# Kernel tuning notes

Hardware: AMD Instinct MI355X
Metric: run time of the kernel (lower is better)

Reference implementation:

```python
import jax, jax.numpy as jnp
import numpy as np
import math

B, N = 1, 768
CS, CZ, CH, H, PQ, PV, E3 = 384, 128, 16, 12, 4, 8, 4
INF, EPS = 1e5, 1e-8


def _quat_to_rot(q):
    # q: [..., 4] unnormalized quaternion -> [..., 3, 3] rotation matrix
    q = q / jnp.linalg.norm(q, axis=-1, keepdims=True)
    w, x, y, z = q[..., 0], q[..., 1], q[..., 2], q[..., 3]
    R = jnp.stack([
        1 - 2 * (y * y + z * z), 2 * (x * y - w * z), 2 * (x * z + w * y),
        2 * (x * y + w * z), 1 - 2 * (x * x + z * z), 2 * (y * z - w * x),
        2 * (x * z - w * y), 2 * (y * z + w * x), 1 - 2 * (x * x + y * y),
    ], axis=-1)
    return R.reshape(q.shape[:-1] + (3, 3))


def setup_inputs() -> dict:
    key = jax.random.key(0)
    ks = jax.random.split(key, 24)
    hc = H * CH
    hpq = H * PQ * 3
    hpkv = H * (PQ + PV) * 3
    cod = CZ // 4 + CH + PV * 4  # 80
    def w(k, shape, fan_in):
        return jax.random.normal(k, shape, jnp.float32) / math.sqrt(fan_in)
    inp = {
        "s": jax.random.normal(ks[0], (B, N, CS), jnp.float32),
        "z": jax.random.normal(ks[1], (B, N, N, CZ), jnp.float32),
        "l1_feats": jax.random.normal(ks[2], (B, N, E3 * 3), jnp.float32),
        "rot": _quat_to_rot(jax.random.normal(ks[3], (B, N, 4), jnp.float32)),
        "trans": jax.random.normal(ks[4], (B, N, 3), jnp.float32),
        "mask": jnp.ones((B, N), jnp.float32),
        "Wq": w(ks[5], (hc, CS), CS), "bq": jnp.zeros((hc,), jnp.float32),
        "Wkv": w(ks[6], (2 * hc, CS), CS), "bkv": jnp.zeros((2 * hc,), jnp.float32),
        "Wqp": w(ks[7], (hpq, CS), CS), "bqp": jnp.zeros((hpq,), jnp.float32),
        "Wkvp": w(ks[8], (hpkv, CS), CS), "bkvp": jnp.zeros((hpkv,), jnp.float32),
        "Wb": w(ks[9], (H, CZ), CZ), "bb": jnp.zeros((H,), jnp.float32),
        "Wdz": w(ks[10], (CZ // 4, CZ), CZ), "bdz": jnp.zeros((CZ // 4,), jnp.float32),
        "Wout": w(ks[11], (CS, H * cod), H * cod), "bout": jnp.zeros((CS,), jnp.float32),
        "Wl1": jax.random.normal(ks[12], (H * PV, E3), jnp.float32),
    }
    return inp


def _split3(x):
    # torch.split(x, d//3, -1) then stack(dim=-1): [..., 3*P] -> [..., P, 3]
    return jnp.swapaxes(x.reshape(x.shape[:-1] + (3, -1)), -1, -2)


def reference(s, z, l1_feats, rot, trans, mask,
              Wq, bq, Wkv, bkv, Wqp, bqp, Wkvp, bkvp,
              Wb, bb, Wdz, bdz, Wout, bout, Wl1):
    s_org = s
    q = (s @ Wq.T + bq).reshape(B, N, H, CH)
    kv = (s @ Wkv.T + bkv).reshape(B, N, H, 2 * CH)
    k, v = kv[..., :CH], kv[..., CH:]

    # points in global frame: R p + t
    q_pts = _split3(s @ Wqp.T + bqp)                      # [B,N,H*PQ,3]
    q_pts = jnp.einsum("bnij,bnpj->bnpi", rot, q_pts) + trans[:, :, None, :]
    q_pts = q_pts.reshape(B, N, H, PQ, 3)
    kv_pts = _split3(s @ Wkvp.T + bkvp)                   # [B,N,H*(PQ+PV),3]
    kv_pts = jnp.einsum("bnij,bnpj->bnpi", rot, kv_pts) + trans[:, :, None, :]
    kv_pts = kv_pts.reshape(B, N, H, PQ + PV, 3)
    k_pts, v_pts = kv_pts[..., :PQ, :], kv_pts[..., PQ:, :]

    b = z @ Wb.T + bb                                     # [B,N,N,H]
    a = math.sqrt(1.0 / (3 * CH)) * jnp.einsum("bihc,bjhc->bhij", q, k)
    a = a + math.sqrt(1.0 / 3) * jnp.transpose(b, (0, 3, 1, 2))

    diff = q_pts[:, :, None] - k_pts[:, None]             # [B,N,N,H,PQ,3]
    pt_att = -0.5 * jnp.sum(diff * diff, axis=(-1, -2))   # [B,N,N,H]
    a = a + jnp.transpose(pt_att, (0, 3, 1, 2))

    sq_mask = INF * (mask[:, :, None] * mask[:, None, :] - 1.0)
    a = jax.nn.softmax(a + sq_mask[:, None], axis=-1)     # [B,H,N,N]

    o = jnp.einsum("bhij,bjhc->bihc", a, v).reshape(B, N, H * CH)
    o_pt = jnp.einsum("bhij,bjhpc->bihpc", a, v_pts)      # [B,N,H,PV,3] (global frame)

    # e3nn o3.Linear on (H*PV)x1o -> E3x1o: per-xyz channel mixing / sqrt(fan_in)
    o_pt_l1 = o_pt.reshape(B, N, H * PV, 3)
    l1_out = l1_feats + (jnp.einsum("bnic,io->bnoc", o_pt_l1, Wl1)
                         / math.sqrt(H * PV)).reshape(B, N, E3 * 3)

    # back to local frame: R^T (p - t)
    o_pt_loc = jnp.einsum("bnji,bnhpj->bnhpi", rot,
                          o_pt - trans[:, :, None, None, :])
    o_pt_dists = jnp.sqrt(jnp.sum(o_pt_loc ** 2, axis=-1) + EPS).reshape(B, N, H * PV)
    o_pt_flat = o_pt_loc.reshape(B, N, H * PV, 3)

    pair_z = z @ Wdz.T + bdz                              # [B,N,N,CZ//4]
    o_pair = jnp.einsum("bhij,bijd->bihd", a, pair_z).reshape(B, N, H * (CZ // 4))

    feats = jnp.concatenate([o, o_pt_flat[..., 0], o_pt_flat[..., 1],
                             o_pt_flat[..., 2], o_pt_dists, o_pair], axis=-1)
    s_out = feats @ Wout.T + bout + s_org
    return s_out, l1_out
```

## Files before the change

### kernel.cpp

```cpp
#include <hip/hip_runtime.h>

#define INFV 100000.0f
#define CQK 0.14433756729740643f
#define CB  0.5773502691896258f
#define INV_SQRT96 0.10206207261596577f

typedef short bf16x8 __attribute__((ext_vector_type(8)));
typedef float f32x4 __attribute__((ext_vector_type(4)));

#define OFF_WT    0
#define OFF_WOT   442368
#define OFF_BU    811008
#define OFF_Q     812160
#define OFF_KH    959616
#define OFF_KPH   1107072
#define OFF_QP    1217664
#define OFF_BM    1328256
#define OFF_A     4867200
#define OFF_VCT   8406144
#define OFF_PZ    8627328
#define OFF_O     18064512
#define OFF_OPT   18211968
#define OFF_OPAIR 18433152
#define OFF_ZB    18728064
#define OFF_WC    18728068
#define OFF_BC    18731140

static __device__ __forceinline__ unsigned short f2bf(float x) {
  unsigned int u = __float_as_uint(x);
  unsigned int r = (u + 0x7fffu + ((u >> 16) & 1u)) >> 16;
  return (unsigned short)r;
}
static __device__ __forceinline__ float bf2f(unsigned short b) {
  return __uint_as_float(((unsigned int)b) << 16);
}

__global__ __launch_bounds__(256) void kT(
    const float* __restrict__ Wq, const float* __restrict__ Wkv,
    const float* __restrict__ Wqp, const float* __restrict__ Wkvp,
    const float* __restrict__ Wout,
    const float* __restrict__ bq, const float* __restrict__ bkv,
    const float* __restrict__ bqp, const float* __restrict__ bkvp,
    const float* __restrict__ Wb, const float* __restrict__ bb,
    const float* __restrict__ Wdz, const float* __restrict__ bdz,
    float* __restrict__ WT, float* __restrict__ WoutT, float* __restrict__ bu,
    unsigned short* __restrict__ vcT, float* __restrict__ zb,
    unsigned short* __restrict__ Wc, float* __restrict__ biasc) {
  int tid = blockIdx.x * 256 + threadIdx.x;
  if (tid < 442368) {
    int f = tid / 1152, u = tid % 1152;
    float w;
    if (u < 192)      w = Wq[u * 384 + f];
    else if (u < 576) w = Wkv[(u - 192) * 384 + f];
    else if (u < 720) w = Wqp[(u - 576) * 384 + f];
    else              w = Wkvp[(u - 720) * 384 + f];
    WT[tid] = w;
  } else if (tid < 811008) {
    int r = tid - 442368;
    int f = r / 384, o = r % 384;
    WoutT[r] = Wout[o * 960 + f];
  } else if (tid < 812160) {
    int u = tid - 811008;
    float bv;
    if (u < 192)      bv = bq[u];
    else if (u < 576) bv = bkv[u - 192];
    else if (u < 720) bv = bqp[u - 576];
    else              bv = bkvp[u - 720];
    bu[u] = bv;
  } else if (tid < 849024) {
    int zid = tid - 812160;
    int h = zid / 3072, r = zid % 3072;
    ((unsigned int*)(vcT + h * 36864 + 40 * 768))[r] = 0u;
  } else if (tid < 849028) {
    ((unsigned int*)zb)[tid - 849024] = 0u;
  } else if (tid < 855172) {
    int wid = tid - 849028;
    int n = wid >> 7, k = wid & 127;
    float val = (n < 12) ? CB * Wb[n * 128 + k] : ((n < 44) ? Wdz[(n - 12) * 128 + k] : 0.f);
    Wc[wid] = f2bf(val);
  } else if (tid < 855220) {
    int n = tid - 855172;
    biasc[n] = (n < 12) ? CB * bb[n] : ((n < 44) ? bdz[n - 12] : 0.f);
  }
}

__global__ __launch_bounds__(384) void kA(
    const float* __restrict__ s, const float* __restrict__ rot, const float* __restrict__ trans,
    const float* __restrict__ WT, const float* __restrict__ bu,
    float* __restrict__ q, float* __restrict__ kh, float* __restrict__ kph,
    float* __restrict__ qp, unsigned short* __restrict__ vcT) {
  __shared__ float sA[4][384];
  __shared__ float praw[4][576];
  const int t = threadIdx.x;
  const int n0 = blockIdx.x * 4;
  for (int idx = t; idx < 4 * 384; idx += 384) sA[idx / 384][idx % 384] = s[n0 * 384 + idx];
  __syncthreads();

  float acc[3][4];
#pragma unroll
  for (int a = 0; a < 3; a++)
#pragma unroll
    for (int r = 0; r < 4; r++) acc[a][r] = 0.f;
  const int u0 = t, u1 = t + 384, u2 = t + 768;

  for (int f = 0; f < 384; f += 4) {
    float4 sr0 = *(const float4*)&sA[0][f];
    float4 sr1 = *(const float4*)&sA[1][f];
    float4 sr2 = *(const float4*)&sA[2][f];
    float4 sr3 = *(const float4*)&sA[3][f];
#pragma unroll
    for (int ff = 0; ff < 4; ff++) {
      const float* wrow = WT + (size_t)(f + ff) * 1152;
      float w0 = wrow[u0], w1 = wrow[u1], w2 = wrow[u2];
      float v0 = ((const float*)&sr0)[ff];
      float v1 = ((const float*)&sr1)[ff];
      float v2 = ((const float*)&sr2)[ff];
      float v3 = ((const float*)&sr3)[ff];
      acc[0][0] = fmaf(w0, v0, acc[0][0]); acc[0][1] = fmaf(w0, v1, acc[0][1]);
      acc[0][2] = fmaf(w0, v2, acc[0][2]); acc[0][3] = fmaf(w0, v3, acc[0][3]);
      acc[1][0] = fmaf(w1, v0, acc[1][0]); acc[1][1] = fmaf(w1, v1, acc[1][1]);
      acc[1][2] = fmaf(w1, v2, acc[1][2]); acc[1][3] = fmaf(w1, v3, acc[1][3]);
      acc[2][0] = fmaf(w2, v0, acc[2][0]); acc[2][1] = fmaf(w2, v1, acc[2][1]);
      acc[2][2] = fmaf(w2, v2, acc[2][2]); acc[2][3] = fmaf(w2, v3, acc[2][3]);
    }
  }

#pragma unroll
  for (int a = 0; a < 3; a++) {
    int u = t + a * 384;
    float bv = bu[u];
#pragma unroll
    for (int r = 0; r < 4; r++) {
      float val = acc[a][r] + bv;
      int n = n0 + r;
      if (u < 192) {
        q[n * 192 + u] = val;
      } else if (u < 576) {
        int l = u - 192, h = l >> 5, rem = l & 31;
        if (rem < 16) kh[h * 12288 + n * 16 + rem] = val;
        else          vcT[h * 36864 + (rem - 16) * 768 + n] = f2bf(val);
      } else {
        praw[r][u - 576] = val;
      }
    }
  }
  __syncthreads();

  for (int task = t; task < 4 * 192; task += 384) {
    int r = task / 192, p = task % 192;
    int n = n0 + r;
    const float* R = rot + n * 9;
    const float* tr = trans + n * 3;
    float x, y, z;
    if (p < 48) {
      x = praw[r][p]; y = praw[r][48 + p]; z = praw[r][96 + p];
      int h = p >> 2, pq = p & 3;
      float* outp = qp + n * 144 + h * 12 + pq * 3;
      outp[0] = R[0] * x + R[1] * y + R[2] * z + tr[0];
      outp[1] = R[3] * x + R[4] * y + R[5] * z + tr[1];
      outp[2] = R[6] * x + R[7] * y + R[8] * z + tr[2];
    } else {
      int pp = p - 48;
      x = praw[r][144 + pp]; y = praw[r][288 + pp]; z = praw[r][432 + pp];
      int h = pp / 12, idx = pp % 12;
      float gx = R[0] * x + R[1] * y + R[2] * z + tr[0];
      float gy = R[3] * x + R[4] * y + R[5] * z + tr[1];
      float gz = R[6] * x + R[7] * y + R[8] * z + tr[2];
      if (idx < 4) {
        float* outp = kph + h * 9216 + n * 12 + idx * 3;
        outp[0] = gx; outp[1] = gy; outp[2] = gz;
      } else {
        int pv = idx - 4;
        unsigned short* vb = vcT + h * 36864 + (16 + pv * 3) * 768 + n;
        vb[0] = f2bf(gx); vb[768] = f2bf(gy); vb[1536] = f2bf(gz);
      }
    }
  }
}

__global__ __launch_bounds__(256) void kB2(
    const float* __restrict__ z, const unsigned short* __restrict__ Wc,
    const float* __restrict__ biasc,
    unsigned short* __restrict__ bm16, unsigned short* __restrict__ pz) {
  __shared__ unsigned short zL[64][136];
  __shared__ unsigned short wL[48][136];
  __shared__ unsigned short oD[64][48];
  __shared__ float biasL[48];
  const int t = threadIdx.x;
  const size_t pid0 = (size_t)blockIdx.x * 64;

  {
    const unsigned int* wsrc = (const unsigned int*)Wc;
#pragma unroll
    for (int it = 0; it < 12; it++) {
      int idx = it * 256 + t;
      int n = idx >> 6, col = (idx & 63) * 2;
      *(unsigned int*)&wL[n][col] = wsrc[idx];
    }
    if (t < 48) biasL[t] = biasc[t];
  }
  const float4* zsrc = (const float4*)(z + pid0 * 128);
#pragma unroll
  for (int it = 0; it < 8; it++) {
    int f4 = it * 256 + t;
    float4 v = zsrc[f4];
    int row = f4 >> 5, col = (f4 & 31) * 4;
    unsigned int p0 = (unsigned int)f2bf(v.x) | ((unsigned int)f2bf(v.y) << 16);
    unsigned int p1 = (unsigned int)f2bf(v.z) | ((unsigned int)f2bf(v.w) << 16);
    uint2 pk = make_uint2(p0, p1);
    *(uint2*)&zL[row][col] = pk;
  }
  __syncthreads();

  const int w = t >> 6, l = t & 63;
  const int lr = l & 15, hk = l >> 4;
  f32x4 acc0 = {0.f, 0.f, 0.f, 0.f}, acc1 = acc0, acc2 = acc0;
  const int arow = w * 16 + lr;
#pragma unroll
  for (int kc = 0; kc < 4; kc++) {
    int col = kc * 32 + hk * 8;
    bf16x8 af = *(const bf16x8*)&zL[arow][col];
    bf16x8 b0 = *(const bf16x8*)&wL[lr][col];
    bf16x8 b1 = *(const bf16x8*)&wL[16 + lr][col];
    bf16x8 b2 = *(const bf16x8*)&wL[32 + lr][col];
    acc0 = __builtin_amdgcn_mfma_f32_16x16x32_bf16(af, b0, acc0, 0, 0, 0);
    acc1 = __builtin_amdgcn_mfma_f32_16x16x32_bf16(af, b1, acc1, 0, 0, 0);
    acc2 = __builtin_amdgcn_mfma_f32_16x16x32_bf16(af, b2, acc2, 0, 0, 0);
  }
  {
    int rb = w * 16 + hk * 4;
#pragma unroll
    for (int r = 0; r < 4; r++) {
      oD[rb + r][lr]      = f2bf(acc0[r] + biasL[lr]);
      oD[rb + r][16 + lr] = f2bf(acc1[r] + biasL[16 + lr]);
      oD[rb + r][32 + lr] = f2bf(acc2[r] + biasL[32 + lr]);
    }
  }
  __syncthreads();

  {
    int row = t >> 2, qd = t & 3;
    uint2 lo = *(const uint2*)&oD[row][12 + qd * 8];
    uint2 hi = *(const uint2*)&oD[row][12 + qd * 8 + 4];
    uint4 val = make_uint4(lo.x, lo.y, hi.x, hi.y);
    *(uint4*)(pz + (pid0 + row) * 32 + qd * 8) = val;
  }
  for (int idx = t; idx < 384; idx += 256) {
    int h = idx / 32, pr = idx % 32;
    unsigned int u = (unsigned int)oD[2 * pr][h] | ((unsigned int)oD[2 * pr + 1][h] << 16);
    ((unsigned int*)(bm16 + (size_t)h * 589824 + pid0))[pr] = u;
  }
}

__global__ __launch_bounds__(256) void kC1(
    const float* __restrict__ q, const float* __restrict__ qp,
    const float* __restrict__ kh, const float* __restrict__ kph,
    const unsigned short* __restrict__ bm16, const float* __restrict__ mask,
    unsigned short* __restrict__ A) {
  __shared__ float lg[12 * 776];
  __shared__ float qL[192], qpL[144], maskL[768];
  __shared__ float mxL[12], ivL[12];
  const int t = threadIdx.x;
  const int i = blockIdx.x;
  for (int idx = t; idx < 192; idx += 256) qL[idx] = q[i * 192 + idx];
  for (int idx = t; idx < 144; idx += 256) qpL[idx] = qp[i * 144 + idx];
  for (int j = t; j < 768; j += 256) maskL[j] = mask[j];
  __syncthreads();
  const float mi = maskL[i];

  for (int h = 0; h < 12; h++) {
    const float4* qv = (const float4*)&qL[h * 16];
    float4 q0 = qv[0], q1 = qv[1], q2 = qv[2], q3 = qv[3];
    const float4* av = (const float4*)&qpL[h * 12];
    float4 a0 = av[0], a1 = av[1], a2 = av[2];
    for (int j = t; j < 768; j += 256) {
      const float4* kr = (const float4*)(kh + h * 12288 + j * 16);
      float4 k0 = kr[0], k1 = kr[1], k2 = kr[2], k3 = kr[3];
      const float4* pr = (const float4*)(kph + h * 9216 + j * 12);
      float4 p0 = pr[0], p1 = pr[1], p2 = pr[2];
      float bsc = bf2f(bm16[(size_t)h * 589824 + i * 768 + j]);
      float qk =
          q0.x * k0.x + q0.y * k0.y + q0.z * k0.z + q0.w * k0.w +
          q1.x * k1.x + q1.y * k1.y + q1.z * k1.z + q1.w * k1.w +
          q2.x * k2.x + q2.y * k2.y + q2.z * k2.z + q2.w * k2.w +
          q3.x * k3.x + q3.y * k3.y + q3.z * k3.z + q3.w * k3.w;
      float d, pt = 0.f;
      d = a0.x - p0.x; pt = fmaf(d, d, pt);
      d = a0.y - p0.y; pt = fmaf(d, d, pt);
      d = a0.z - p0.z; pt = fmaf(d, d, pt);
      d = a0.w - p0.w; pt = fmaf(d, d, pt);
      d = a1.x - p1.x; pt = fmaf(d, d, pt);
      d = a1.y - p1.y; pt = fmaf(d, d, pt);
      d = a1.z - p1.z; pt = fmaf(d, d, pt);
      d = a1.w - p1.w; pt = fmaf(d, d, pt);
      d = a2.x - p2.x; pt = fmaf(d, d, pt);
      d = a2.y - p2.y; pt = fmaf(d, d, pt);
      d = a2.z - p2.z; pt = fmaf(d, d, pt);
      d = a2.w - p2.w; pt = fmaf(d, d, pt);
      lg[h * 776 + j] = fmaf(CQK, qk, bsc) - 0.5f * pt + INFV * (mi * maskL[j] - 1.0f);
    }
  }
  __syncthreads();

  const int w = t >> 6, ln = t & 63;
  for (int h = w; h < 12; h += 4) {
    const float* row = lg + h * 776;
    float m = -3.0e38f;
#pragma unroll
    for (int kq = 0; kq < 12; kq++) m = fmaxf(m, row[ln + kq * 64]);
#pragma unroll
    for (int sh = 1; sh < 64; sh <<= 1) m = fmaxf(m, __shfl_xor(m, sh));
    float ssum = 0.f;
#pragma unroll
    for (int kq = 0; kq < 12; kq++) ssum += __expf(row[ln + kq * 64] - m);
#pragma unroll
    for (int sh = 1; sh < 64; sh <<= 1) ssum += __shfl_xor(ssum, sh);
    if (ln == 0) { mxL[h] = m; ivL[h] = 1.0f / ssum; }
  }
  __syncthreads();

  for (int idx = t; idx < 4608; idx += 256) {
    int h = idx / 384, jp = idx % 384;
    float m = mxL[h], iv = ivL[h];
    int j0 = jp * 2;
    float e0 = __expf(lg[h * 776 + j0] - m) * iv;
    float e1 = __expf(lg[h * 776 + j0 + 1] - m) * iv;
    unsigned int pk = (unsigned int)f2bf(e0) | ((unsigned int)f2bf(e1) << 16);
    ((unsigned int*)(A + (size_t)h * 589824 + i * 768))[jp] = pk;
  }
}

__global__ __launch_bounds__(128) void kC2(
    const unsigned short* __restrict__ A, const unsigned short* __restrict__ vcT,
    float* __restrict__ o_out, float* __restrict__ opt_out) {
  const int t = threadIdx.x;
  const int h = blockIdx.x % 12, it = blockIdx.x / 12;
  const int i0 = it * 32;
  const int w = t >> 6, l = t & 63;
  const int lr = l & 15, lk = (l >> 4) * 8;
  f32x4 acc0 = {0.f, 0.f, 0.f, 0.f}, acc1 = acc0, acc2 = acc0;
  const unsigned short* ab = A + (size_t)h * 589824 + (i0 + w * 16 + lr) * 768 + lk;
  const unsigned short* bb = vcT + h * 36864 + lr * 768 + lk;
#pragma unroll 4
  for (int kc = 0; kc < 24; kc++) {
    int k0 = kc * 32;
    bf16x8 avf = *(const bf16x8*)(ab + k0);
    bf16x8 b0 = *(const bf16x8*)(bb + k0);
    bf16x8 b1 = *(const bf16x8*)(bb + 16 * 768 + k0);
    bf16x8 b2 = *(const bf16x8*)(bb + 32 * 768 + k0);
    acc0 = __builtin_amdgcn_mfma_f32_16x16x32_bf16(avf, b0, acc0, 0, 0, 0);
    acc1 = __builtin_amdgcn_mfma_f32_16x16x32_bf16(avf, b1, acc1, 0, 0, 0);
    acc2 = __builtin_amdgcn_mfma_f32_16x16x32_bf16(avf, b2, acc2, 0, 0, 0);
  }
  const int rowb = i0 + w * 16 + (l >> 4) * 4;
#pragma unroll
  for (int r = 0; r < 4; r++) {
    int row = rowb + r;
    o_out[row * 192 + h * 16 + lr] = acc0[r];
    opt_out[row * 288 + h * 24 + lr] = acc1[r];
    if (lr < 8) opt_out[row * 288 + h * 24 + 16 + lr] = acc2[r];
  }
}

__global__ __launch_bounds__(256) void kC3(
    const unsigned short* __restrict__ A, const unsigned short* __restrict__ pz,
    const unsigned short* __restrict__ zb, float* __restrict__ opair_out) {
  __shared__ unsigned short pzT[32 * 776];
  __shared__ float red[4][16][33];
  const int t = threadIdx.x, i = blockIdx.x;

  unsigned int* pzU = (unsigned int*)pzT;
  for (int p = t; p < 384; p += 256) {
    const uint4* r0 = (const uint4*)(pz + (size_t)(i * 768 + 2 * p) * 32);
    union { uint4 v[8]; unsigned short u[64]; } rw;
#pragma unroll
    for (int c = 0; c < 8; c++) rw.v[c] = r0[c];
#pragma unroll
    for (int d = 0; d < 32; d++)
      pzU[d * 388 + p] = (unsigned int)rw.u[d] | ((unsigned int)rw.u[32 + d] << 16);
  }
  __syncthreads();

  const int w = t >> 6, l = t & 63;
  const int lr = l & 15, lk = (l >> 4) * 8;
  f32x4 acc0 = {0.f, 0.f, 0.f, 0.f}, acc1 = acc0;
  const unsigned short* abase = (lr < 12) ? (A + (size_t)lr * 589824 + i * 768 + lk) : zb;
  const int astep = (lr < 12) ? 1 : 0;
#pragma unroll
  for (int kc = 0; kc < 6; kc++) {
    int k0 = w * 192 + kc * 32;
    bf16x8 avf = *(const bf16x8*)(abase + astep * k0);
    bf16x8 b0 = *(const bf16x8*)(pzT + lr * 776 + k0 + lk);
    bf16x8 b1 = *(const bf16x8*)(pzT + (16 + lr) * 776 + k0 + lk);
    acc0 = __builtin_amdgcn_mfma_f32_16x16x32_bf16(avf, b0, acc0, 0, 0, 0);
    acc1 = __builtin_amdgcn_mfma_f32_16x16x32_bf16(avf, b1, acc1, 0, 0, 0);
  }
#pragma unroll
  for (int r = 0; r < 4; r++) {
    red[w][(l >> 4) * 4 + r][lr] = acc0[r];
    red[w][(l >> 4) * 4 + r][16 + lr] = acc1[r];
  }
  __syncthreads();
  for (int idx = t; idx < 512; idx += 256) {
    int row = idx >> 5, col = idx & 31;
    if (row < 12) {
      float sv = red[0][row][col] + red[1][row][col] + red[2][row][col] + red[3][row][col];
      opair_out[i * 384 + row * 32 + col] = sv;
    }
  }
}

__global__ __launch_bounds__(512) void kD(
    const float* __restrict__ o_in, const float* __restrict__ opt_in, const float* __restrict__ opair_in,
    const float* __restrict__ rot, const float* __restrict__ trans,
    const float* __restrict__ l1f, const float* __restrict__ Wl1,
    const float* __restrict__ WoutT, const float* __restrict__ bout,
    const float* __restrict__ s_org, float* __restrict__ out) {
  __shared__ float feats[4][960];
  __shared__ float part[2][256][6];
  const int t = threadIdx.x;
  const int n0 = blockIdx.x * 4;

  for (int idx = t; idx < 768; idx += 512) feats[idx / 192][idx % 192] = o_in[n0 * 192 + idx];
  for (int idx = t; idx < 1536; idx += 512) feats[idx / 384][576 + idx % 384] = opair_in[n0 * 384 + idx];
  if (t < 384) {
    int r = t / 96, p = t % 96, n = n0 + r;
    float x = opt_in[n * 288 + p * 3 + 0];
    float y = opt_in[n * 288 + p * 3 + 1];
    float zc = opt_in[n * 288 + p * 3 + 2];
    const float* R = rot + n * 9;
    const float* tr = trans + n * 3;
    float dx = x - tr[0], dy = y - tr[1], dz = zc - tr[2];
    float l0 = R[0] * dx + R[3] * dy + R[6] * dz;
    float l1 = R[1] * dx + R[4] * dy + R[7] * dz;
    float l2 = R[2] * dx + R[5] * dy + R[8] * dz;
    feats[r][192 + p] = l0;
    feats[r][288 + p] = l1;
    feats[r][384 + p] = l2;
    feats[r][480 + p] = sqrtf(l0 * l0 + l1 * l1 + l2 * l2 + 1e-8f);
  } else if (t < 432) {
    int tt = t - 384, r = tt / 12, lq = tt % 12, n = n0 + r;
    int oo = lq / 3, cc = lq % 3;
    float acc = 0.f;
    for (int i = 0; i < 96; i++) acc = fmaf(opt_in[n * 288 + i * 3 + cc], Wl1[i * 4 + oo], acc);
    out[294912 + n * 12 + lq] = l1f[n * 12 + lq] + acc * INV_SQRT96;
  }
  __syncthreads();

  const int fh = t >> 8, tt = t & 255;
  const int o0 = tt & 127, rp = tt >> 7;
  float acc[3][2] = {{0.f, 0.f}, {0.f, 0.f}, {0.f, 0.f}};
  for (int f = fh * 480; f < fh * 480 + 480; f++) {
    float w0 = WoutT[f * 384 + o0];
    float w1 = WoutT[f * 384 + o0 + 128];
    float w2 = WoutT[f * 384 + o0 + 256];
    float s0 = feats[rp * 2][f], s1 = feats[rp * 2 + 1][f];
    acc[0][0] = fmaf(w0, s0, acc[0][0]); acc[0][1] = fmaf(w0, s1, acc[0][1]);
    acc[1][0] = fmaf(w1, s0, acc[1][0]); acc[1][1] = fmaf(w1, s1, acc[1][1]);
    acc[2][0] = fmaf(w2, s0, acc[2][0]); acc[2][1] = fmaf(w2, s1, acc[2][1]);
  }
#pragma unroll
  for (int kq = 0; kq < 3; kq++)
#pragma unroll
    for (int r = 0; r < 2; r++) part[fh][tt][kq * 2 + r] = acc[kq][r];
  __syncthreads();
  if (t < 256) {
    const int ob = t & 127, rb = t >> 7;
#pragma unroll
    for (int kq = 0; kq < 3; kq++) {
      int o = ob + kq * 128;
#pragma unroll
      for (int r = 0; r < 2; r++) {
        int n = n0 + rb * 2 + r;
        float v = part[0][t][kq * 2 + r] + part[1][t][kq * 2 + r] + bout[o] + s_org[n * 384 + o];
        out[n * 384 + o] = v;
      }
    }
  }
}

extern "C" void kernel_launch(void* const* d_in, const int* in_sizes, int n_in,
                              void* d_out, int out_size, void* d_ws, size_t ws_size,
                              hipStream_t stream) {
  (void)in_sizes; (void)n_in; (void)out_size; (void)ws_size;
  const float* s     = (const float*)d_in[0];
  const float* z     = (const float*)d_in[1];
  const float* l1f   = (const float*)d_in[2];
  const float* rot   = (const float*)d_in[3];
  const float* trans = (const float*)d_in[4];
  const float* mask  = (const float*)d_in[5];
  const float* Wq    = (const float*)d_in[6];
  const float* bq    = (const float*)d_in[7];
  const float* Wkv   = (const float*)d_in[8];
  const float* bkv   = (const float*)d_in[9];
  const float* Wqp   = (const float*)d_in[10];
  const float* bqp   = (const float*)d_in[11];
  const float* Wkvp  = (const float*)d_in[12];
  const float* bkvp  = (const float*)d_in[13];
  const float* Wb    = (const float*)d_in[14];
  const float* bb    = (const float*)d_in[15];
  const float* Wdz   = (const float*)d_in[16];
  const float* bdz   = (const float*)d_in[17];
  const float* Wout  = (const float*)d_in[18];
  const float* bout  = (const float*)d_in[19];
  const float* Wl1   = (const float*)d_in[20];
  float* out = (float*)d_out;
  float* ws  = (float*)d_ws;

  float* WT    = ws + OFF_WT;
  float* WoutT = ws + OFF_WOT;
  float* bu    = ws + OFF_BU;
  float* qb    = ws + OFF_Q;
  float* khb   = ws + OFF_KH;
  float* kphb  = ws + OFF_KPH;
  float* qpb   = ws + OFF_QP;
  unsigned short* bm16 = (unsigned short*)(ws + OFF_BM);
  unsigned short* Ab   = (unsigned short*)(ws + OFF_A);
  unsigned short* vcT  = (unsigned short*)(ws + OFF_VCT);
  unsigned short* pzb  = (unsigned short*)(ws + OFF_PZ);
  float* ob    = ws + OFF_O;
  float* optb  = ws + OFF_OPT;
  float* opairb= ws + OFF_OPAIR;
  float* zbf   = ws + OFF_ZB;
  unsigned short* Wc = (unsigned short*)(ws + OFF_WC);
  float* biasc = ws + OFF_BC;

  kT<<<3342, 256, 0, stream>>>(Wq, Wkv, Wqp, Wkvp, Wout, bq, bkv, bqp, bkvp,
                               Wb, bb, Wdz, bdz,
                               WT, WoutT, bu, vcT, zbf, Wc, biasc);
  kA<<<192, 384, 0, stream>>>(s, rot, trans, WT, bu, qb, khb, kphb, qpb, vcT);
  kB2<<<9216, 256, 0, stream>>>(z, Wc, biasc, bm16, pzb);
  kC1<<<768, 256, 0, stream>>>(qb, qpb, khb, kphb, bm16, mask, Ab);
  kC2<<<288, 128, 0, stream>>>(Ab, vcT, ob, optb);
  kC3<<<768, 256, 0, stream>>>(Ab, pzb, (const unsigned short*)zbf, opairb);
  kD<<<192, 512, 0, stream>>>(ob, optb, opairb, rot, trans, l1f, Wl1, WoutT, bout, s, out);
}
```

Before: 262.2 us.

## Compute attention logits with bf16 MFMA using expanded point-distance dot products

New measurement: 232.4 us. 11.4% less time.

```diff
diff --git a/kernel.cpp b/kernel.cpp
--- a/kernel.cpp
+++ b/kernel.cpp
@@ -2,6 +2,7 @@
 
 #define INFV 100000.0f
 #define CQK 0.14433756729740643f
+#define SQCQK 0.3799178428257963f
 #define CB  0.5773502691896258f
 #define INV_SQRT96 0.10206207261596577f
 
@@ -11,10 +12,6 @@
 #define OFF_WT    0
 #define OFF_WOT   442368
 #define OFF_BU    811008
-#define OFF_Q     812160
-#define OFF_KH    959616
-#define OFF_KPH   1107072
-#define OFF_QP    1217664
 #define OFF_BM    1328256
 #define OFF_A     4867200
 #define OFF_VCT   8406144
@@ -25,6 +22,9 @@
 #define OFF_ZB    18728064
 #define OFF_WC    18728068
 #define OFF_BC    18731140
+#define OFF_QC    18731200
+#define OFF_KC    19026112
+#define OFF_SQK   19321024
 
 static __device__ __forceinline__ unsigned short f2bf(float x) {
   unsigned int u = __float_as_uint(x);
@@ -87,10 +87,11 @@
 __global__ __launch_bounds__(384) void kA(
     const float* __restrict__ s, const float* __restrict__ rot, const float* __restrict__ trans,
     const float* __restrict__ WT, const float* __restrict__ bu,
-    float* __restrict__ q, float* __restrict__ kh, float* __restrict__ kph,
-    float* __restrict__ qp, unsigned short* __restrict__ vcT) {
+    unsigned short* __restrict__ qc, unsigned short* __restrict__ kc,
+    float* __restrict__ sqk, unsigned short* __restrict__ vcT) {
   __shared__ float sA[4][384];
   __shared__ float praw[4][576];
+  __shared__ float sqp[4][12][4];
   const int t = threadIdx.x;
   const int n0 = blockIdx.x * 4;
   for (int idx = t; idx < 4 * 384; idx += 384) sA[idx / 384][idx % 384] = s[n0 * 384 + idx];
@@ -134,10 +135,11 @@
       float val = acc[a][r] + bv;
       int n = n0 + r;
       if (u < 192) {
-        q[n * 192 + u] = val;
+        int h = u >> 4, c = u & 15;
+        qc[((size_t)(h * 768) + n) * 64 + c] = f2bf(SQCQK * val);
       } else if (u < 576) {
-        int l = u - 192, h = l >> 5, rem = l & 31;
-        if (rem < 16) kh[h * 12288 + n * 16 + rem] = val;
+        int l2 = u - 192, h = l2 >> 5, rem = l2 & 31;
+        if (rem < 16) kc[((size_t)(h * 768) + n) * 64 + rem] = f2bf(SQCQK * val);
         else          vcT[h * 36864 + (rem - 16) * 768 + n] = f2bf(val);
       } else {
         praw[r][u - 576] = val;
@@ -146,35 +148,60 @@
   }
   __syncthreads();
 
-  for (int task = t; task < 4 * 192; task += 384) {
-    int r = task / 192, p = task % 192;
+  for (int task = t; task < 768; task += 384) {
+    int r = task / 192, rem = task % 192;
+    int h = rem >> 4, pidx = rem & 15;
     int n = n0 + r;
     const float* R = rot + n * 9;
     const float* tr = trans + n * 3;
     float x, y, z;
-    if (p < 48) {
+    if (pidx < 4) {
+      int p = h * 4 + pidx;
       x = praw[r][p]; y = praw[r][48 + p]; z = praw[r][96 + p];
-      int h = p >> 2, pq = p & 3;
-      float* outp = qp + n * 144 + h * 12 + pq * 3;
-      outp[0] = R[0] * x + R[1] * y + R[2] * z + tr[0];
-      outp[1] = R[3] * x + R[4] * y + R[5] * z + tr[1];
-      outp[2] = R[6] * x + R[7] * y + R[8] * z + tr[2];
     } else {
-      int pp = p - 48;
+      int pp = h * 12 + (pidx - 4);
       x = praw[r][144 + pp]; y = praw[r][288 + pp]; z = praw[r][432 + pp];
-      int h = pp / 12, idx = pp % 12;
-      float gx = R[0] * x + R[1] * y + R[2] * z + tr[0];
-      float gy = R[3] * x + R[4] * y + R[5] * z + tr[1];
-      float gz = R[6] * x + R[7] * y + R[8] * z + tr[2];
-      if (idx < 4) {
-        float* outp = kph + h * 9216 + n * 12 + idx * 3;
-        outp[0] = gx; outp[1] = gy; outp[2] = gz;
-      } else {
-        int pv = idx - 4;
-        unsigned short* vb = vcT + h * 36864 + (16 + pv * 3) * 768 + n;
-        vb[0] = f2bf(gx); vb[768] = f2bf(gy); vb[1536] = f2bf(gz);
+    }
+    float g0 = R[0] * x + R[1] * y + R[2] * z + tr[0];
+    float g1 = R[3] * x + R[4] * y + R[5] * z + tr[1];
+    float g2 = R[6] * x + R[7] * y + R[8] * z + tr[2];
+    if (pidx < 4) {
+      unsigned short* base = qc + ((size_t)(h * 768) + n) * 64;
+      int d0 = 16 + pidx * 3;
+      float g[3] = {g0, g1, g2};
+#pragma unroll
+      for (int c = 0; c < 3; c++) {
+        unsigned short hi = f2bf(g[c]);
+        unsigned short lo = f2bf(g[c] - bf2f(hi));
+        base[d0 + c] = hi; base[12 + d0 + c] = lo; base[24 + d0 + c] = hi;
       }
-    }
+    } else if (pidx < 8) {
+      unsigned short* base = kc + ((size_t)(h * 768) + n) * 64;
+      int d0 = 16 + (pidx - 4) * 3;
+      float g[3] = {g0, g1, g2};
+#pragma unroll
+      for (int c = 0; c < 3; c++) {
+        unsigned short hi = f2bf(g[c]);
+        unsigned short lo = f2bf(g[c] - bf2f(hi));
+        base[d0 + c] = hi; base[12 + d0 + c] = hi; base[24 + d0 + c] = lo;
+      }
+      sqp[r][h][pidx - 4] = g0 * g0 + g1 * g1 + g2 * g2;
+    } else {
+      int pv = pidx - 8;
+      unsigned short* vb = vcT + h * 36864 + (16 + pv * 3) * 768 + n;
+      vb[0] = f2bf(g0); vb[768] = f2bf(g1); vb[1536] = f2bf(g2);
+    }
+  }
+  for (int task = t; task < 576; task += 384) {
+    int r = task / 144, rem = task % 144;
+    int h = rem / 12, c = rem % 12;
+    size_t off = ((size_t)(h * 768) + n0 + r) * 64 + 52 + c;
+    qc[off] = 0; kc[off] = 0;
+  }
+  __syncthreads();
+  if (t < 48) {
+    int r = t / 12, h = t % 12;
+    sqk[h * 768 + n0 + r] = sqp[r][h][0] + sqp[r][h][1] + sqp[r][h][2] + sqp[r][h][3];
   }
 }
 
@@ -252,81 +279,69 @@
   }
 }
 
-__global__ __launch_bounds__(256) void kC1(
-    const float* __restrict__ q, const float* __restrict__ qp,
-    const float* __restrict__ kh, const float* __restrict__ kph,
-    const unsigned short* __restrict__ bm16, const float* __restrict__ mask,
-    unsigned short* __restrict__ A) {
-  __shared__ float lg[12 * 776];
-  __shared__ float qL[192], qpL[144], maskL[768];
-  __shared__ float mxL[12], ivL[12];
+__global__ __launch_bounds__(256) void kC1M(
+    const unsigned short* __restrict__ qc, const unsigned short* __restrict__ kc,
+    const float* __restrict__ sqk, const unsigned short* __restrict__ bm16,
+    const float* __restrict__ mask, unsigned short* __restrict__ A) {
+  __shared__ float lg[16 * 780];
   const int t = threadIdx.x;
-  const int i = blockIdx.x;
-  for (int idx = t; idx < 192; idx += 256) qL[idx] = q[i * 192 + idx];
-  for (int idx = t; idx < 144; idx += 256) qpL[idx] = qp[i * 144 + idx];
-  for (int j = t; j < 768; j += 256) maskL[j] = mask[j];
-  __syncthreads();
-  const float mi = maskL[i];
-
-  for (int h = 0; h < 12; h++) {
-    const float4* qv = (const float4*)&qL[h * 16];
-    float4 q0 = qv[0], q1 = qv[1], q2 = qv[2], q3 = qv[3];
-    const float4* av = (const float4*)&qpL[h * 12];
-    float4 a0 = av[0], a1 = av[1], a2 = av[2];
-    for (int j = t; j < 768; j += 256) {
-      const float4* kr = (const float4*)(kh + h * 12288 + j * 16);
-      float4 k0 = kr[0], k1 = kr[1], k2 = kr[2], k3 = kr[3];
-      const float4* pr = (const float4*)(kph + h * 9216 + j * 12);
-      float4 p0 = pr[0], p1 = pr[1], p2 = pr[2];
-      float bsc = bf2f(bm16[(size_t)h * 589824 + i * 768 + j]);
-      float qk =
-          q0.x * k0.x + q0.y * k0.y + q0.z * k0.z + q0.w * k0.w +
-          q1.x * k1.x + q1.y * k1.y + q1.z * k1.z + q1.w * k1.w +
-          q2.x * k2.x + q2.y * k2.y + q2.z * k2.z + q2.w * k2.w +
-          q3.x * k3.x + q3.y * k3.y + q3.z * k3.z + q3.w * k3.w;
-      float d, pt = 0.f;
-      d = a0.x - p0.x; pt = fmaf(d, d, pt);
-      d = a0.y - p0.y; pt = fmaf(d, d, pt);
-      d = a0.z - p0.z; pt = fmaf(d, d, pt);
-      d = a0.w - p0.w; pt = fmaf(d, d, pt);
-      d = a1.x - p1.x; pt = fmaf(d, d, pt);
-      d = a1.y - p1.y; pt = fmaf(d, d, pt);
-      d = a1.z - p1.z; pt = fmaf(d, d, pt);
-      d = a1.w - p1.w; pt = fmaf(d, d, pt);
-      d = a2.x - p2.x; pt = fmaf(d, d, pt);
-      d = a2.y - p2.y; pt = fmaf(d, d, pt);
-      d = a2.z - p2.z; pt = fmaf(d, d, pt);
-      d = a2.w - p2.w; pt = fmaf(d, d, pt);
-      lg[h * 776 + j] = fmaf(CQK, qk, bsc) - 0.5f * pt + INFV * (mi * maskL[j] - 1.0f);
-    }
-  }
-  __syncthreads();
-
-  const int w = t >> 6, ln = t & 63;
-  for (int h = w; h < 12; h += 4) {
-    const float* row = lg + h * 776;
+  const int h = blockIdx.x % 12, it = blockIdx.x / 12;
+  const int i0 = it * 16;
+  const int w = t >> 6, l = t & 63;
+  const int lr = l & 15, hk = l >> 4;
+
+  const unsigned short* qrow = qc + ((size_t)(h * 768) + i0 + lr) * 64 + hk * 8;
+  bf16x8 a0 = *(const bf16x8*)(qrow);
+  bf16x8 a1 = *(const bf16x8*)(qrow + 32);
+  float miA[4];
+#pragma unroll
+  for (int r = 0; r < 4; r++) miA[r] = mask[i0 + hk * 4 + r];
+
+  for (int q = 0; q < 12; q++) {
+    int j0 = (w * 12 + q) * 16;
+    const unsigned short* krow = kc + ((size_t)(h * 768) + j0 + lr) * 64 + hk * 8;
+    bf16x8 b0 = *(const bf16x8*)(krow);
+    bf16x8 b1 = *(const bf16x8*)(krow + 32);
+    f32x4 acc = {0.f, 0.f, 0.f, 0.f};
+    acc = __builtin_amdgcn_mfma_f32_16x16x32_bf16(a0, b0, acc, 0, 0, 0);
+    acc = __builtin_amdgcn_mfma_f32_16x16x32_bf16(a1, b1, acc, 0, 0, 0);
+    int j = j0 + lr;
+    float skj = 0.5f * sqk[h * 768 + j];
+    float mj = mask[j];
+    const unsigned short* bmc = bm16 + (size_t)h * 589824 + (size_t)(i0 + hk * 4) * 768 + j;
+#pragma unroll
+    for (int r = 0; r < 4; r++) {
+      int ii = hk * 4 + r;
+      float bsc = bf2f(bmc[r * 768]);
+      lg[ii * 780 + j] = acc[r] - skj + bsc + INFV * (miA[r] * mj - 1.0f);
+    }
+  }
+  __syncthreads();
+
+  const int ln = l;
+#pragma unroll
+  for (int rr = 0; rr < 4; rr++) {
+    int row = w * 4 + rr;
+    float* rowp = lg + row * 780;
     float m = -3.0e38f;
 #pragma unroll
-    for (int kq = 0; kq < 12; kq++) m = fmaxf(m, row[ln + kq * 64]);
+    for (int kq = 0; kq < 12; kq++) m = fmaxf(m, rowp[ln + kq * 64]);
 #pragma unroll
     for (int sh = 1; sh < 64; sh <<= 1) m = fmaxf(m, __shfl_xor(m, sh));
     float ssum = 0.f;
 #pragma unroll
-    for (int kq = 0; kq < 12; kq++) ssum += __expf(row[ln + kq * 64] - m);
+    for (int kq = 0; kq < 12; kq++) ssum += __expf(rowp[ln + kq * 64] - m);
 #pragma unroll
     for (int sh = 1; sh < 64; sh <<= 1) ssum += __shfl_xor(ssum, sh);
-    if (ln == 0) { mxL[h] = m; ivL[h] = 1.0f / ssum; }
-  }
-  __syncthreads();
-
-  for (int idx = t; idx < 4608; idx += 256) {
-    int h = idx / 384, jp = idx % 384;
-    float m = mxL[h], iv = ivL[h];
-    int j0 = jp * 2;
-    float e0 = __expf(lg[h * 776 + j0] - m) * iv;
-    float e1 = __expf(lg[h * 776 + j0 + 1] - m) * iv;
-    unsigned int pk = (unsigned int)f2bf(e0) | ((unsigned int)f2bf(e1) << 16);
-    ((unsigned int*)(A + (size_t)h * 589824 + i * 768))[jp] = pk;
+    float iv = 1.0f / ssum;
+    unsigned int* arow = (unsigned int*)(A + (size_t)h * 589824 + (size_t)(i0 + row) * 768);
+#pragma unroll
+    for (int kq = 0; kq < 6; kq++) {
+      int jp = ln + kq * 64;
+      float e0 = __expf(rowp[2 * jp] - m) * iv;
+      float e1 = __expf(rowp[2 * jp + 1] - m) * iv;
+      arow[jp] = (unsigned int)f2bf(e0) | ((unsigned int)f2bf(e1) << 16);
+    }
   }
 }
 
@@ -510,10 +525,6 @@
   float* WT    = ws + OFF_WT;
   float* WoutT = ws + OFF_WOT;
   float* bu    = ws + OFF_BU;
-  float* qb    = ws + OFF_Q;
-  float* khb   = ws + OFF_KH;
-  float* kphb  = ws + OFF_KPH;
-  float* qpb   = ws + OFF_QP;
   unsigned short* bm16 = (unsigned short*)(ws + OFF_BM);
   unsigned short* Ab   = (unsigned short*)(ws + OFF_A);
   unsigned short* vcT  = (unsigned short*)(ws + OFF_VCT);
@@ -524,13 +535,16 @@
   float* zbf   = ws + OFF_ZB;
   unsigned short* Wc = (unsigned short*)(ws + OFF_WC);
   float* biasc = ws + OFF_BC;
+  unsigned short* qcb = (unsigned short*)(ws + OFF_QC);
+  unsigned short* kcb = (unsigned short*)(ws + OFF_KC);
+  float* sqkb = ws + OFF_SQK;
 
   kT<<<3342, 256, 0, stream>>>(Wq, Wkv, Wqp, Wkvp, Wout, bq, bkv, bqp, bkvp,
                                Wb, bb, Wdz, bdz,
                                WT, WoutT, bu, vcT, zbf, Wc, biasc);
-  kA<<<192, 384, 0, stream>>>(s, rot, trans, WT, bu, qb, khb, kphb, qpb, vcT);
+  kA<<<192, 384, 0, stream>>>(s, rot, trans, WT, bu, qcb, kcb, sqkb, vcT);
   kB2<<<9216, 256, 0, stream>>>(z, Wc, biasc, bm16, pzb);
-  kC1<<<768, 256, 0, stream>>>(qb, qpb, khb, kphb, bm16, mask, Ab);
+  kC1M<<<576, 256, 0, stream>>>(qcb, kcb, sqkb, bm16, mask, Ab);
   kC2<<<288, 128, 0, stream>>>(Ab, vcT, ob, optb);
   kC3<<<768, 256, 0, stream>>>(Ab, pzb, (const unsigned short*)zbf, opairb);
   kD<<<192, 512, 0, stream>>>(ob, optb, opairb, rot, trans, l1f, Wl1, WoutT, bout, s, out);
```
